# Kernel optimization log

Measured on AMD Instinct MI355X. Metric: run time of the kernel, lower is better.

## Reference

```python
import jax, jax.numpy as jnp
import numpy as np

N, E, G = 16384, 65536, 512
T, FIN, FOUT = 4, 128, 32
_DEG_HIST = np.array([1.0, 2.0, 3.0, 4.0])
AVG_LOG = float((np.log(np.arange(4) + 1.0) * _DEG_HIST).sum() / _DEG_HIST.sum())


def _bn(x, g, b, eps=1e-5):
    # BatchNorm1d in training mode: biased batch stats
    m = x.mean(0)
    v = x.var(0)
    return (x - m) * jax.lax.rsqrt(v + eps) * g + b


def _pna_conv(x, edge_index, ea_raw, We_c, be_c, Wpre, bpre, Wpost, bpost, Wlin, blin):
    src, dst = edge_index[0], edge_index[1]
    ea = ea_raw @ We_c + be_c                                   # conv-internal edge encoder [E,FIN]
    xt = jnp.broadcast_to(x[:, None, :], (N, T, FIN))           # towers share input (divide_input=False)
    h = jnp.concatenate([xt[dst], xt[src],
                         jnp.broadcast_to(ea[:, None, :], (E, T, FIN))], axis=-1)  # [E,T,3*FIN]
    m = jnp.einsum('etf,tfg->etg', h, Wpre) + bpre              # per-tower pre-NN [E,T,FIN]
    deg = jnp.clip(jax.ops.segment_sum(jnp.ones((E,), x.dtype), dst, N), 1.0)
    inv = (1.0 / deg)[:, None, None]
    mean = jax.ops.segment_sum(m, dst, N) * inv
    mean2 = jax.ops.segment_sum(m * m, dst, N) * inv
    std = jnp.sqrt(jax.nn.relu(mean2 - mean * mean) + 1e-5)
    mn = jax.ops.segment_min(m, dst, N)
    mx = jax.ops.segment_max(m, dst, N)
    mn = jnp.where(jnp.isfinite(mn), mn, 0.0)
    mx = jnp.where(jnp.isfinite(mx), mx, 0.0)
    agg = jnp.concatenate([mean, mn, mx, std], axis=-1)         # [N,T,4*FIN]
    s = (jnp.log(deg + 1.0) / AVG_LOG)[:, None, None]           # amplification scaler
    out = jnp.concatenate([agg, agg * s, agg / s], axis=-1)     # identity|amp|attenuation [N,T,12*FIN]
    out = jnp.concatenate([xt, out], axis=-1)                   # [N,T,13*FIN]
    out = jnp.einsum('ntf,tfg->ntg', out, Wpost) + bpost        # per-tower post-NN [N,T,FOUT]
    return out.reshape(N, T * FOUT) @ Wlin + blin               # tower mixing [N,FIN]


def setup_inputs() -> dict:
    key = jax.random.key(0)
    ks = jax.random.split(key, 24)
    def rn(k, shape, scale=0.05):
        return jax.random.normal(k, shape, dtype=jnp.float32) * scale
    return dict(
        x=jax.random.normal(ks[0], (N, 11), jnp.float32),
        edge_attr=jax.random.uniform(ks[1], (E, 4), jnp.float32),
        edge_index=jax.random.randint(ks[2], (2, E), 0, N),
        batch=jnp.sort(jax.random.randint(ks[3], (N,), 0, G)),
        Wa=rn(ks[4], (11, FIN), 0.2), ba=rn(ks[5], (FIN,)),
        We=rn(ks[6], (4, FIN), 0.2), be=rn(ks[7], (FIN,)),
        We_conv=rn(ks[8], (3, FIN, FIN)), be_conv=rn(ks[9], (3, FIN)),
        Wpre=rn(ks[10], (3, T, 3 * FIN, FIN)), bpre=rn(ks[11], (3, T, FIN)),
        Wpost=rn(ks[12], (3, T, 13 * FIN, FOUT)), bpost=rn(ks[13], (3, T, FOUT)),
        Wlin=rn(ks[14], (3, FIN, FIN)), blin=rn(ks[15], (3, FIN)),
        bng=1.0 + rn(ks[16], (3, FIN)), bnb=rn(ks[17], (3, FIN)),
        W1=rn(ks[18], (FIN, 64), 0.1), b1=rn(ks[19], (64,)),
        hg=1.0 + rn(ks[20], (64,)), hb=rn(ks[21], (64,)),
        W2=rn(ks[22], (64, 1), 0.1), b2=rn(ks[23], (1,)),
    )


def reference(x, edge_attr, edge_index, batch, Wa, ba, We, be,
              We_conv, be_conv, Wpre, bpre, Wpost, bpost, Wlin, blin,
              bng, bnb, W1, b1, hg, hb, W2, b2):
    h = jax.nn.relu(x @ Wa + ba)
    ea = jax.nn.relu(edge_attr @ We + be)
    for l in range(3):
        h = jax.nn.relu(_bn(_pna_conv(h, edge_index, ea, We_conv[l], be_conv[l],
                                      Wpre[l], bpre[l], Wpost[l], bpost[l],
                                      Wlin[l], blin[l]), bng[l], bnb[l]))
    cnt = jnp.clip(jax.ops.segment_sum(jnp.ones((N,), h.dtype), batch, G), 1.0)
    pooled = jax.ops.segment_sum(h, batch, G) / cnt[:, None]    # global_mean_pool
    z = jax.nn.relu(pooled @ W1 + b1)
    z = _bn(z, hg, hb)
    return (z @ W2 + b2).reshape(-1)
```

## Files before the change

kernel.cpp:

```cpp
#include <hip/hip_runtime.h>
#include <hip/hip_bf16.h>

#define DEVFN static __device__ __forceinline__

constexpr int NN = 16384;
constexpr int EE = 65536;
constexpr int GG = 512;
constexpr float AVG_LOG_F = 1.0227308671603782f;

typedef _Float16 hfrag __attribute__((ext_vector_type(8)));
typedef __attribute__((ext_vector_type(4))) float f4;

DEVFN unsigned short f2h(float f) {
  _Float16 h = (_Float16)f;
  unsigned short r; __builtin_memcpy(&r, &h, 2); return r;
}
DEVFN float h2f(unsigned short s) {
  _Float16 h; __builtin_memcpy(&h, &s, 2); return (float)h;
}

DEVFN float4 ld4hf(const unsigned short* p) {
  ushort4 u = *(const ushort4*)p;
  float4 r;
  r.x = h2f(u.x); r.y = h2f(u.y); r.z = h2f(u.z); r.w = h2f(u.w);
  return r;
}

DEVFN int swk(int row, int k) {
  return (k & ~31) + ((((k >> 3) & 3) ^ ((row >> 1) & 3)) << 3) + (k & 7);
}

DEVFN void gll16(const unsigned short* g, unsigned short* l) {
  __builtin_amdgcn_global_load_lds(
      (__attribute__((address_space(1))) void*)g,
      (__attribute__((address_space(3))) void*)l, 16, 0, 0);
}

struct AuxP {
  const float* p0;
  const float* p1;
  const float* p2;
  const float* p3;
  const float* p4;
};

template <int ASRC, int NT, bool BIAS, bool RELU, bool OHALF>
__global__ __launch_bounds__(256) void mgemm(
    const void* __restrict__ Av, const unsigned short* __restrict__ WT,
    const float* __restrict__ bias,
    float* __restrict__ C, AuxP aux,
    int Nc, int K, int lda, int ldc,
    long long bsA, long long bsW, long long bsC, int bsBias)
{
  constexpr bool COPYA = (ASRC == 1);
  constexpr int BST = NT * 16 * 32;

  const int z = blockIdx.z;
  WT += (long long)z * bsW;
  if (BIAS) bias += (long long)z * bsBias;
  float* Cf = C + (OHALF ? 0 : (long long)z * bsC);
  unsigned short* Cu = (unsigned short*)C + (OHALF ? (long long)z * bsC : 0);

  __shared__ __align__(16) unsigned short AhS[2 * 128 * 32];
  __shared__ __align__(16) unsigned short BhS[2 * BST];

  const int tid = threadIdx.x;
  const long long bm = (long long)blockIdx.x * 128;
  const int bn = blockIdx.y * (NT * 16);
  const int w = tid >> 6;
  const int lane = tid & 63;
  const int quad = lane >> 4;
  const int c16 = lane & 15;
  const int srow = lane >> 2;
  const int sslot = (lane & 3) << 3;

  const int arow = tid >> 1;
  const int sel = tid & 1;
  const long long rowsrc = bm + arow;

  f4 acc[2][NT];
#pragma unroll
  for (int mt = 0; mt < 2; ++mt)
#pragma unroll
    for (int nt = 0; nt < NT; ++nt) acc[mt][nt] = (f4){0.f, 0.f, 0.f, 0.f};

  const unsigned short* whp = WT + (long long)(bn + srow) * K + sslot;

  const unsigned short* ahp = nullptr;
  if (COPYA || ASRC == 3)
    ahp = (const unsigned short*)Av + (long long)z * bsA + (bm + srow) * (long long)lda + sslot;

  float invdc = 1.f;
  float sv = 0.f, iv = 0.f;
  const float* apA = nullptr;
  const float* Prow_base = nullptr;
  if (ASRC == 3) {
    Prow_base = aux.p0 + rowsrc * 384;
    sv = aux.p2[rowsrc];
    iv = aux.p3[rowsrc];
  } else if (ASRC == 4) {
    apA = (const float*)Av + (long long)z * bsA + rowsrc * lda;
    invdc = 1.f / fmaxf(aux.p0[rowsrc], 1.f);
  }
  const int swa = (arow >> 1) & 3;
  const int s0us = arow * 32 + (((2 * sel) ^ swa) << 3);
  const int s1us = arow * 32 + (((2 * sel + 1) ^ swa) << 3);

  const int swr8 = ((quad ^ ((c16 >> 1) & 3)) << 3);

  auto stageB = [&](int bi, int k0) {
#pragma unroll
    for (int ch = w; ch < NT; ch += 4)
      gll16(whp + (long long)ch * 16 * K + k0, BhS + bi * BST + ch * 512);
  };
  auto stageA = [&](int bi, int k0) {
#pragma unroll
    for (int ch = w; ch < 8; ch += 4)
      gll16(ahp + (long long)ch * 16 * lda + k0, AhS + bi * 4096 + ch * 512);
  };
  auto stageLoad = [&](int k0, float* va) {
    const int ck0 = k0 + sel * 16;
    if (ASRC == 3) {
      const float* Prow = Prow_base + ((ck0 >> 5) * 96) + (ck0 & 31);
#pragma unroll
      for (int i = 0; i < 16; ++i)
        va[i] = Prow[i] + sv * Prow[32 + i] + iv * Prow[64 + i] + aux.p4[ck0 + i];
    } else {
      *(float4*)&va[0] = *(const float4*)(apA + ck0);
      *(float4*)&va[4] = *(const float4*)(apA + ck0 + 4);
      *(float4*)&va[8] = *(const float4*)(apA + ck0 + 8);
      *(float4*)&va[12] = *(const float4*)(apA + ck0 + 12);
    }
  };
  auto stageWrite = [&](int bi, const float* va) {
    hfrag hv0, hv1;
#pragma unroll
    for (int i = 0; i < 16; ++i) {
      float x = va[i];
      if (ASRC == 4) x *= invdc;
      if (i < 8) hv0[i] = (_Float16)x;
      else       hv1[i - 8] = (_Float16)x;
    }
    *(hfrag*)&AhS[bi * 4096 + s0us] = hv0;
    *(hfrag*)&AhS[bi * 4096 + s1us] = hv1;
  };
  auto fragmfma = [&](int bi) {
    hfrag ah[2];
#pragma unroll
    for (int mt = 0; mt < 2; ++mt) {
      const int r = w * 32 + mt * 16 + c16;
      ah[mt] = *(const hfrag*)&AhS[bi * 4096 + r * 32 + swr8];
    }
#pragma unroll
    for (int nt = 0; nt < NT; ++nt) {
      const int r = nt * 16 + c16;
      hfrag bh = *(const hfrag*)&BhS[bi * BST + r * 32 + swr8];
#pragma unroll
      for (int mt = 0; mt < 2; ++mt)
        acc[mt][nt] = __builtin_amdgcn_mfma_f32_16x16x32_f16(ah[mt], bh, acc[mt][nt], 0, 0, 0);
    }
  };

  float va[16];
  const int nk = K >> 5;

  if (COPYA) {
    stageA(0, 0);
    stageB(0, 0);
  } else {
    stageLoad(0, va);
    stageB(0, 0);
    stageWrite(0, va);
  }
  __syncthreads();

  for (int kt = 0; kt < nk; ++kt) {
    const int bi = kt & 1;
    const bool pf = (kt + 1 < nk);
    bool nextds = false;
    if (pf) {
      const int k0 = (kt + 1) << 5;
      stageB(bi ^ 1, k0);
      if (COPYA) {
        stageA(bi ^ 1, k0);
      } else if (ASRC == 3 && k0 >= 128) {
        stageA(bi ^ 1, k0 - 128);
      } else {
        stageLoad(k0, va);
        nextds = true;
      }
    }
    fragmfma(bi);
    if (nextds) stageWrite(bi ^ 1, va);
    __syncthreads();
  }

  float ls[NT], lq[NT];
#pragma unroll
  for (int nt = 0; nt < NT; ++nt) { ls[nt] = 0.f; lq[nt] = 0.f; }
#pragma unroll
  for (int nt = 0; nt < NT; ++nt) {
    int col = bn + nt * 16 + c16;
    if (col >= Nc) continue;
    float bv = BIAS ? bias[col] : 0.f;
#pragma unroll
    for (int mt = 0; mt < 2; ++mt) {
#pragma unroll
      for (int r = 0; r < 4; ++r) {
        long long row = bm + w * 32 + mt * 16 + quad * 4 + r;
        float v = acc[mt][nt][r] + bv;
        if (RELU) v = fmaxf(v, 0.f);
        if (ASRC == 3) { ls[nt] += v; lq[nt] += v * v; }
        if (OHALF) Cu[row * ldc + col] = f2h(v);
        else Cf[row * ldc + col] = v;
      }
    }
  }
  if constexpr (ASRC == 3) {
    float* csum = (float*)AhS;
    float* csq = csum + 128;
    if (tid < 256 && tid >= 128) {}
    if (tid < 128) { csum[tid] = 0.f; csq[tid] = 0.f; }
    __syncthreads();
#pragma unroll
    for (int nt = 0; nt < NT; ++nt) {
      int col = bn + nt * 16 + c16;
      atomicAdd(&csum[col], ls[nt]);
      atomicAdd(&csq[col], lq[nt]);
    }
    __syncthreads();
    float* colsum = (float*)aux.p1;
    if (tid < 128) {
      atomicAdd(&colsum[tid], csum[tid]);
      atomicAdd(&colsum[128 + tid], csq[tid]);
    }
  }
}

__global__ void node_enc(const float* __restrict__ x, const float* __restrict__ Wa,
                         const float* __restrict__ ba, unsigned short* __restrict__ hb)
{
  int n = blockIdx.x, c = threadIdx.x;
  float acc = ba[c];
#pragma unroll
  for (int k = 0; k < 11; ++k) acc += x[n * 11 + k] * Wa[k * 128 + c];
  hb[((long long)n << 7) + swk(n, c)] = f2h(fmaxf(acc, 0.f));
}

__global__ void edge_enc(const float* __restrict__ eat, const float* __restrict__ We,
                         const float* __restrict__ be, const int* __restrict__ slot_of,
                         unsigned short* __restrict__ ef)
{
  int e = blockIdx.x, c = threadIdx.x;
  float acc = be[c];
#pragma unroll
  for (int k = 0; k < 4; ++k) acc += eat[e * 4 + k] * We[k * 128 + c];
  long long slot = slot_of[e];
  ef[slot * 128 + swk((int)slot, c)] = f2h(fmaxf(acc, 0.f));
}

__global__ void count_deg(const int* __restrict__ dst, int* __restrict__ degi)
{
  int e = blockIdx.x * 256 + threadIdx.x;
  if (e < EE) atomicAdd(&degi[dst[e]], 1);
}

__global__ __launch_bounds__(1024) void scan_k(const int* __restrict__ degi,
                                               int* __restrict__ row_off,
                                               int* __restrict__ cursor,
                                               float* __restrict__ s_arr,
                                               float* __restrict__ invs)
{
  __shared__ int tsum[1024];
  int t = threadIdx.x;
  int local[16];
  int base = t * 16;
  int s = 0;
#pragma unroll
  for (int i = 0; i < 16; ++i) { local[i] = s; s += degi[base + i]; }
  tsum[t] = s;
  __syncthreads();
  for (int off = 1; off < 1024; off <<= 1) {
    int v = (t >= off) ? tsum[t - off] : 0;
    __syncthreads();
    tsum[t] += v;
    __syncthreads();
  }
  int prev = (t == 0) ? 0 : tsum[t - 1];
#pragma unroll
  for (int i = 0; i < 16; ++i) {
    int start = prev + local[i];
    row_off[base + i] = start;
    cursor[base + i] = start;
    int cnt = degi[base + i];
    float degc = fmaxf((float)cnt, 1.f);
    float sv = logf(degc + 1.f) / AVG_LOG_F;
    s_arr[base + i] = sv;
    invs[base + i] = 1.f / sv;
  }
  if (t == 1023) row_off[NN] = tsum[1023];
}

__global__ void scatter_k(const int* __restrict__ src, const int* __restrict__ dst,
                          int* __restrict__ cursor,
                          int* __restrict__ slot_of, int* __restrict__ esrc)
{
  int e = blockIdx.x * 256 + threadIdx.x;
  if (e >= EE) return;
  int d = dst[e];
  int slot = atomicAdd(&cursor[d], 1);
  slot_of[e] = slot;
  esrc[slot] = src[e];
}

__global__ __launch_bounds__(512) void fold_w(const float* __restrict__ We_conv,
                                              const float* __restrict__ Wpre,
                                              float* __restrict__ Wfold)
{
  int k = blockIdx.x & 127, l = blockIdx.x >> 7;
  int t = threadIdx.x >> 7, f = threadIdx.x & 127;
  const float* wc = We_conv + (long long)(l * 128 + k) * 128;
  const float* wp = Wpre + ((long long)((l * 4 + t) * 384 + 256)) * 128 + f;
  float acc = 0.f;
  for (int j = 0; j < 128; ++j) acc += wc[j] * wp[(long long)j * 128];
  Wfold[((long long)(l * 128 + k)) * 512 + threadIdx.x] = acc;
}

__global__ __launch_bounds__(512) void fold_b(const float* __restrict__ be_conv,
                                              const float* __restrict__ Wpre,
                                              const float* __restrict__ bpre,
                                              float* __restrict__ bfold)
{
  int l = blockIdx.x;
  int t = threadIdx.x >> 7, f = threadIdx.x & 127;
  const float* bc = be_conv + l * 128;
  const float* wp = Wpre + ((long long)((l * 4 + t) * 384 + 256)) * 128 + f;
  float acc = bpre[(l * 4 + t) * 128 + f];
  for (int j = 0; j < 128; ++j) acc += bc[j] * wp[(long long)j * 128];
  bfold[l * 512 + threadIdx.x] = acc;
}

__global__ __launch_bounds__(128) void pack_all(
    const float* __restrict__ Wpre, const float* __restrict__ WfoldF,
    const float* __restrict__ Wpost, const float* __restrict__ Wlin,
    const float* __restrict__ W1,
    unsigned short* __restrict__ preABT, unsigned short* __restrict__ foldT,
    unsigned short* __restrict__ post3T, unsigned short* __restrict__ linT2,
    unsigned short* __restrict__ w1T)
{
  const int b = blockIdx.x;
  const int t = threadIdx.x;
  if (b < 3072) {
    int lt = b >> 8, n = b & 255, k = t;
    int row = (n < 128) ? k : (128 + k);
    int f = n & 127;
    float v = Wpre[((long long)(lt * 384 + row)) * 128 + f];
    preABT[((long long)(lt * 256 + n)) * 128 + swk(n, k)] = f2h(v);
  } else if (b < 4608) {
    int b2 = b - 3072;
    int lt = b2 >> 7, n = b2 & 127, k = t;
    int l = lt >> 2, tw = lt & 3;
    float v = WfoldF[((long long)(l * 128 + k)) * 512 + tw * 128 + n];
    foldT[((long long)(lt * 128 + n)) * 128 + swk(n, k)] = f2h(v);
  } else if (b < 6144) {
    int b3 = b - 4608;
    int lt = b3 >> 7, c = b3 & 127;
#pragma unroll
    for (int j = 0; j < 4; ++j) {
      int r = t + 128 * j;
      float v = 0.f;
      if (c < 96)
        v = Wpost[((long long)(lt * 1664 + 128 + (c >> 5) * 512 + r)) * 32 + (c & 31)];
      post3T[((long long)(lt * 128 + c)) * 512 + swk(c, r)] = f2h(v);
    }
  } else if (b < 6528) {
    int b4 = b - 6144;
    int l = b4 >> 7, n = b4 & 127, k = t;
    float v = Wlin[((long long)(l * 128 + k)) * 128 + n];
    linT2[((long long)(l * 128 + n)) * 256 + swk(n, k)] = f2h(v);
  } else if (b < 6912) {
    int b5 = b - 6528;
    int l = b5 >> 7, kk = b5 & 127, o = t;
    float acc = 0.f;
    for (int c = 0; c < 128; ++c) {
      float wx = Wpost[((long long)((l * 4 + (c >> 5)) * 1664 + kk)) * 32 + (c & 31)];
      acc += wx * Wlin[((long long)(l * 128 + c)) * 128 + o];
    }
    linT2[((long long)(l * 128 + o)) * 256 + swk(o, 128 + kk)] = f2h(acc);
  } else {
    int n = b - 6912, k = t;
    w1T[(long long)n * 128 + swk(n, k)] = f2h(W1[k * 64 + n]);
  }
}

__global__ __launch_bounds__(256) void aggregate_ct(
    const unsigned short* __restrict__ ABb, const unsigned short* __restrict__ Mb,
    const int* __restrict__ row_off, const int* __restrict__ esrc,
    unsigned short* __restrict__ aggs)
{
  const int tid = threadIdx.x;
  const int c4 = (tid & 31) << 2;
  const int z = (tid >> 5) & 3;
  const int n = blockIdx.x * 2 + (tid >> 7);
  const unsigned short* M = Mb + (long long)z * EE * 128;
  const unsigned short* ABs = ABb + (long long)z * NN * 256;
  unsigned short* ag = aggs + (long long)z * NN * 512;
  const int beg = row_off[n], end = row_off[n + 1];
  const int cnt = end - beg;
  const float degc = fmaxf((float)cnt, 1.0f);
  const float4 aval = ld4hf(&ABs[(long long)n * 256 + c4]);

  float sum[4] = {0.f, 0.f, 0.f, 0.f}, sq[4] = {0.f, 0.f, 0.f, 0.f};
  float mn[4] = {INFINITY, INFINITY, INFINITY, INFINITY};
  float mx[4] = {-INFINITY, -INFINITY, -INFINITY, -INFINITY};

  auto upd = [&](const float4& mv, const float4& bv) {
    float m0 = aval.x + bv.x + mv.x;
    float m1 = aval.y + bv.y + mv.y;
    float m2 = aval.z + bv.z + mv.z;
    float m3 = aval.w + bv.w + mv.w;
    sum[0] += m0; sq[0] += m0 * m0; mn[0] = fminf(mn[0], m0); mx[0] = fmaxf(mx[0], m0);
    sum[1] += m1; sq[1] += m1 * m1; mn[1] = fminf(mn[1], m1); mx[1] = fmaxf(mx[1], m1);
    sum[2] += m2; sq[2] += m2 * m2; mn[2] = fminf(mn[2], m2); mx[2] = fmaxf(mx[2], m2);
    sum[3] += m3; sq[3] += m3 * m3; mn[3] = fminf(mn[3], m3); mx[3] = fmaxf(mx[3], m3);
  };

  for (int s0 = beg; s0 < end; s0 += 4) {
    const int e1 = min(s0 + 1, end - 1);
    const int e2 = min(s0 + 2, end - 1);
    const int e3 = min(s0 + 3, end - 1);
    const int sA = esrc[s0], sB = esrc[e1], sC = esrc[e2], sD = esrc[e3];
    const float4 mA = ld4hf(&M[(long long)s0 * 128 + c4]);
    const float4 mB = ld4hf(&M[(long long)e1 * 128 + c4]);
    const float4 mC = ld4hf(&M[(long long)e2 * 128 + c4]);
    const float4 mD = ld4hf(&M[(long long)e3 * 128 + c4]);
    const float4 bA = ld4hf(&ABs[(long long)sA * 256 + 128 + c4]);
    const float4 bB = ld4hf(&ABs[(long long)sB * 256 + 128 + c4]);
    const float4 bC = ld4hf(&ABs[(long long)sC * 256 + 128 + c4]);
    const float4 bD = ld4hf(&ABs[(long long)sD * 256 + 128 + c4]);
    upd(mA, bA);
    if (s0 + 1 < end) upd(mB, bB);
    if (s0 + 2 < end) upd(mC, bC);
    if (s0 + 3 < end) upd(mD, bD);
  }

  const float inv = 1.0f / degc;
  float mean[4], stdv[4];
#pragma unroll
  for (int j = 0; j < 4; ++j) {
    mean[j] = sum[j] * inv;
    float var = sq[j] * inv - mean[j] * mean[j];
    stdv[j] = sqrtf(fmaxf(var, 0.f) + 1e-5f);
    if (cnt == 0) { mn[j] = 0.f; mx[j] = 0.f; }
  }
  const int sc = swk(n, c4);
  const long long base = (long long)n * 512 + sc;
  ushort4 o;
  o.x = f2h(mean[0]); o.y = f2h(mean[1]); o.z = f2h(mean[2]); o.w = f2h(mean[3]);
  *(ushort4*)&ag[base] = o;
  o.x = f2h(mn[0]); o.y = f2h(mn[1]); o.z = f2h(mn[2]); o.w = f2h(mn[3]);
  *(ushort4*)&ag[base + 128] = o;
  o.x = f2h(mx[0]); o.y = f2h(mx[1]); o.z = f2h(mx[2]); o.w = f2h(mx[3]);
  *(ushort4*)&ag[base + 256] = o;
  o.x = f2h(stdv[0]); o.y = f2h(stdv[1]); o.z = f2h(stdv[2]); o.w = f2h(stdv[3]);
  *(ushort4*)&ag[base + 384] = o;
}

__global__ void bn_coef(const float* __restrict__ colsum, const float* __restrict__ colsq,
                        const float* __restrict__ g, const float* __restrict__ b,
                        float* __restrict__ coef)
{
  int c = threadIdx.x;
  float mean = colsum[c] * (1.f / 16384.f);
  float var = colsq[c] * (1.f / 16384.f) - mean * mean;
  float sc = g[c] * rsqrtf(var + 1e-5f);
  coef[c] = sc;
  coef[128 + c] = b[c] - mean * sc;
}

__global__ __launch_bounds__(256) void bn_apply(const float* __restrict__ y,
                                                const float* __restrict__ coef,
                                                unsigned short* __restrict__ hb)
{
  int idx = blockIdx.x * 256 + threadIdx.x;
  int c = idx & 127, n = idx >> 7;
  float v = fmaxf(y[idx] * coef[c] + coef[128 + c], 0.f);
  hb[((long long)n << 7) + swk(n, c)] = f2h(v);
}

__global__ void pool_add(const float* __restrict__ y, const float* __restrict__ colsum,
                         const float* __restrict__ colsq, const float* __restrict__ g,
                         const float* __restrict__ b, const int* __restrict__ batch,
                         float* __restrict__ pooled, float* __restrict__ cntf)
{
  int n = blockIdx.x, c = threadIdx.x;
  float mean = colsum[c] * (1.f / 16384.f);
  float var = colsq[c] * (1.f / 16384.f) - mean * mean;
  float v = fmaxf((y[(long long)n * 128 + c] - mean) * rsqrtf(var + 1e-5f) * g[c] + b[c], 0.f);
  int bb = batch[n];
  atomicAdd(&pooled[(long long)bb * 128 + c], v);
  if (c == 0) atomicAdd(&cntf[bb], 1.f);
}

__global__ __launch_bounds__(256) void zstats(const float* __restrict__ z,
                                              float* __restrict__ zm, float* __restrict__ zv)
{
  int j = blockIdx.x;
  float s = 0.f, q = 0.f;
  for (int g = threadIdx.x; g < GG; g += 256) {
    float v = z[g * 64 + j];
    s += v;
    q += v * v;
  }
  __shared__ float ps[256], pq[256];
  ps[threadIdx.x] = s;
  pq[threadIdx.x] = q;
  __syncthreads();
  for (int st = 128; st > 0; st >>= 1) {
    if (threadIdx.x < st) {
      ps[threadIdx.x] += ps[threadIdx.x + st];
      pq[threadIdx.x] += pq[threadIdx.x + st];
    }
    __syncthreads();
  }
  if (threadIdx.x == 0) {
    float m = ps[0] / (float)GG;
    zm[j] = m;
    zv[j] = pq[0] / (float)GG - m * m;
  }
}

__global__ void final_out(const float* __restrict__ z, const float* __restrict__ zm,
                          const float* __restrict__ zv, const float* __restrict__ hg,
                          const float* __restrict__ hb, const float* __restrict__ W2,
                          const float* __restrict__ b2, float* __restrict__ out)
{
  int g = blockIdx.x;
  int j = threadIdx.x;
  float v = (z[g * 64 + j] - zm[j]) * rsqrtf(zv[j] + 1e-5f) * hg[j] + hb[j];
  float t = v * W2[j];
#pragma unroll
  for (int off = 32; off > 0; off >>= 1) t += __shfl_down(t, off);
  if (j == 0) out[g] = t + b2[0];
}

extern "C" void kernel_launch(void* const* d_in, const int* in_sizes, int n_in,
                              void* d_out, int out_size, void* d_ws, size_t ws_size,
                              hipStream_t stream)
{
  (void)in_sizes; (void)n_in; (void)out_size;
  const float* x = (const float*)d_in[0];
  const float* eat = (const float*)d_in[1];
  const int* ei = (const int*)d_in[2];
  const int* batch = (const int*)d_in[3];
  const float* Wa = (const float*)d_in[4];
  const float* ba = (const float*)d_in[5];
  const float* We = (const float*)d_in[6];
  const float* be = (const float*)d_in[7];
  const float* We_conv = (const float*)d_in[8];
  const float* be_conv = (const float*)d_in[9];
  const float* Wpre = (const float*)d_in[10];
  const float* bpre = (const float*)d_in[11];
  const float* Wpost = (const float*)d_in[12];
  const float* bpost = (const float*)d_in[13];
  const float* Wlin = (const float*)d_in[14];
  const float* blin = (const float*)d_in[15];
  const float* bng = (const float*)d_in[16];
  const float* bnb = (const float*)d_in[17];
  const float* W1 = (const float*)d_in[18];
  const float* b1 = (const float*)d_in[19];
  const float* hg = (const float*)d_in[20];
  const float* hb = (const float*)d_in[21];
  const float* W2 = (const float*)d_in[22];
  const float* b2 = (const float*)d_in[23];
  float* out = (float*)d_out;

  const int* srcI = ei;
  const int* dstI = ei + EE;

  char* ws = (char*)d_ws;
  size_t off = 0;
  auto alloc = [&](size_t bytes) -> char* {
    char* p = ws + off;
    off += (bytes + 255) & ~(size_t)255;
    return p;
  };

  unsigned short* hbf = (unsigned short*)alloc((size_t)NN * 128 * 2);
  float* hn = (float*)alloc((size_t)NN * 128 * 4);
  unsigned short* eaf = (unsigned short*)alloc((size_t)EE * 128 * 2);
  unsigned short* AB = (unsigned short*)alloc((size_t)4 * NN * 256 * 2);
  char* Mregion = alloc((size_t)4 * EE * 128 * 2);
  unsigned short* Mb = (unsigned short*)Mregion;
  float* P = (float*)Mregion;
  unsigned short* aggt = (unsigned short*)alloc((size_t)4 * NN * 512 * 2);
  float* s_arr = (float*)alloc((size_t)NN * 4);
  float* invs = (float*)alloc((size_t)NN * 4);
  int* degi = (int*)alloc((size_t)NN * 4);
  int* cursor = (int*)alloc((size_t)NN * 4);
  int* row_off = (int*)alloc((size_t)(NN + 1) * 4);
  int* slot_of = (int*)alloc((size_t)EE * 4);
  int* esrc = (int*)alloc((size_t)EE * 4);
  float* WfoldF = (float*)alloc((size_t)3 * 128 * 512 * 4);
  float* bfold = (float*)alloc((size_t)3 * 512 * 4);
  unsigned short* preABT = (unsigned short*)alloc((size_t)12 * 256 * 128 * 2);
  unsigned short* foldT = (unsigned short*)alloc((size_t)12 * 128 * 128 * 2);
  unsigned short* post3T = (unsigned short*)alloc((size_t)12 * 128 * 512 * 2);
  unsigned short* linT2 = (unsigned short*)alloc((size_t)3 * 128 * 256 * 2);
  unsigned short* w1T = (unsigned short*)alloc((size_t)64 * 128 * 2);
  float* colstats = (float*)alloc(512 * 4);
  float* bncoef = (float*)alloc(256 * 4);
  float* pooled = (float*)alloc((size_t)GG * 128 * 4);
  float* cntf = (float*)alloc((size_t)GG * 4);
  float* zbuf = (float*)alloc((size_t)GG * 64 * 4);
  float* zm = (float*)alloc(64 * 4);
  float* zv = (float*)alloc(64 * 4);

  if (off > ws_size) return;

  float* cs[2] = {colstats, colstats + 256};

  hipMemsetAsync(degi, 0, (size_t)NN * 4, stream);
  count_deg<<<EE / 256, 256, 0, stream>>>(dstI, degi);
  scan_k<<<1, 1024, 0, stream>>>(degi, row_off, cursor, s_arr, invs);
  scatter_k<<<EE / 256, 256, 0, stream>>>(srcI, dstI, cursor, slot_of, esrc);

  node_enc<<<NN, 128, 0, stream>>>(x, Wa, ba, hbf);
  edge_enc<<<EE, 128, 0, stream>>>(eat, We, be, slot_of, eaf);
  fold_w<<<384, 512, 0, stream>>>(We_conv, Wpre, WfoldF);
  fold_b<<<3, 512, 0, stream>>>(be_conv, Wpre, bpre, bfold);
  pack_all<<<6976, 128, 0, stream>>>(Wpre, WfoldF, Wpost, Wlin, W1,
                                     preABT, foldT, post3T, linT2, w1T);

  for (int l = 0; l < 3; ++l) {
    hipMemsetAsync(cs[l & 1], 0, 256 * 4, stream);
    mgemm<1, 8, false, false, true><<<dim3(NN / 128, 2, 4), 256, 0, stream>>>(
        hbf, preABT + (size_t)l * 4 * 256 * 128, nullptr, (float*)AB, AuxP{},
        256, 128, 128, 256, 0, (long long)256 * 128, (long long)NN * 256, 0);
    mgemm<1, 8, true, false, true><<<dim3(EE / 128, 1, 4), 256, 0, stream>>>(
        eaf, foldT + (size_t)l * 4 * 128 * 128, bfold + l * 512, (float*)Mb, AuxP{},
        128, 128, 128, 128, 0, (long long)128 * 128, (long long)EE * 128, 128);
    aggregate_ct<<<dim3(NN / 2, 1, 1), 256, 0, stream>>>(AB, Mb, row_off, esrc, aggt);
    mgemm<1, 6, false, false, false><<<dim3(NN / 128, 1, 4), 256, 0, stream>>>(
        aggt, post3T + (size_t)l * 4 * 128 * 512, nullptr, P, AuxP{},
        96, 512, 512, 384, (long long)NN * 512, (long long)128 * 512, 96, 0);
    mgemm<3, 8, true, false, false><<<dim3(NN / 128, 1, 1), 256, 0, stream>>>(
        hbf, linT2 + (size_t)l * 128 * 256, blin + l * 128, hn,
        AuxP{P, cs[l & 1], s_arr, invs, bpost + l * 128},
        128, 256, 128, 128, 0, 0, 0, 0);
    if (l < 2) {
      bn_coef<<<1, 128, 0, stream>>>(cs[l & 1], cs[l & 1] + 128,
                                     bng + l * 128, bnb + l * 128, bncoef);
      bn_apply<<<NN * 128 / 256, 256, 0, stream>>>(hn, bncoef, hbf);
    }
  }

  hipMemsetAsync(pooled, 0, (size_t)GG * 128 * 4, stream);
  hipMemsetAsync(cntf, 0, (size_t)GG * 4, stream);
  pool_add<<<NN, 128, 0, stream>>>(hn, cs[0], cs[0] + 128,
                                   bng + 2 * 128, bnb + 2 * 128, batch, pooled, cntf);
  mgemm<4, 4, true, true, false><<<dim3(GG / 128, 1, 1), 256, 0, stream>>>(
      pooled, w1T, b1, zbuf, AuxP{cntf, nullptr, nullptr, nullptr, nullptr},
      64, 128, 128, 64, 0, 0, 0, 0);
  zstats<<<64, 256, 0, stream>>>(zbuf, zm, zv);
  final_out<<<GG, 64, 0, stream>>>(zbuf, zm, zv, hg, hb, W2, b2, out);
}
```

Baseline: 596.7 us.

## Merge pre-GEMMs, fold node encoder into pack, store intermediates in fp16, inline BN coef

Combines the node-projection and edge-projection GEMMs of each layer into one launch (abc_gemm) with a block-index split. Moves the node encoder into the pack_all kernel and packs two edges per block in edge_enc. Stores the post-GEMM output P and the layer output hn as fp16 instead of fp32, which halves that traffic. Also computes the BN coefficients inside bn_apply and zeroes all colstats with a single memset, removing kernel launches. The fp16 intermediates add rounding error before batch norm.

After: 570.0 us. 1.05x faster.

```diff
diff --git a/kernel.cpp b/kernel.cpp
--- a/kernel.cpp
+++ b/kernel.cpp
@@ -43,6 +43,102 @@
   const float* p3;
   const float* p4;
 };
+
+__global__ __launch_bounds__(256) void abc_gemm(
+    const unsigned short* __restrict__ hbf, const unsigned short* __restrict__ preABT_l,
+    unsigned short* __restrict__ AB,
+    const unsigned short* __restrict__ eaf, const unsigned short* __restrict__ foldT_l,
+    const float* __restrict__ bfold_l, unsigned short* __restrict__ Mb)
+{
+  __shared__ __align__(16) unsigned short AhS[2 * 4096];
+  __shared__ __align__(16) unsigned short BhS[2 * 4096];
+
+  const int bid = blockIdx.x;
+  const unsigned short* Abase;
+  const unsigned short* Wbase;
+  const float* bias = nullptr;
+  unsigned short* Cu;
+  int ldc, bn;
+  long long bm;
+  if (bid < 1024) {
+    const int z = bid >> 8, y = (bid >> 7) & 1, xm = bid & 127;
+    Abase = hbf;
+    Wbase = preABT_l + (size_t)z * 256 * 128;
+    Cu = AB + (size_t)z * NN * 256;
+    ldc = 256; bn = y * 128; bm = (long long)xm * 128;
+  } else {
+    const int idx = bid - 1024;
+    const int z = idx >> 9, xm = idx & 511;
+    Abase = eaf;
+    Wbase = foldT_l + (size_t)z * 128 * 128;
+    bias = bfold_l + z * 128;
+    Cu = Mb + (size_t)z * EE * 128;
+    ldc = 128; bn = 0; bm = (long long)xm * 128;
+  }
+
+  const int tid = threadIdx.x;
+  const int w = tid >> 6;
+  const int lane = tid & 63;
+  const int quad = lane >> 4;
+  const int c16 = lane & 15;
+  const int srow = lane >> 2;
+  const int sslot = (lane & 3) << 3;
+
+  f4 acc[2][8];
+#pragma unroll
+  for (int mt = 0; mt < 2; ++mt)
+#pragma unroll
+    for (int nt = 0; nt < 8; ++nt) acc[mt][nt] = (f4){0.f, 0.f, 0.f, 0.f};
+
+  const unsigned short* whp = Wbase + (long long)(bn + srow) * 128 + sslot;
+  const unsigned short* ahp = Abase + (bm + srow) * 128 + sslot;
+  const int swr8 = ((quad ^ ((c16 >> 1) & 3)) << 3);
+
+  auto stage = [&](int bi, int k0) {
+#pragma unroll
+    for (int ch = w; ch < 8; ch += 4) {
+      gll16(ahp + (long long)ch * 16 * 128 + k0, AhS + bi * 4096 + ch * 512);
+      gll16(whp + (long long)ch * 16 * 128 + k0, BhS + bi * 4096 + ch * 512);
+    }
+  };
+  auto fragmfma = [&](int bi) {
+    hfrag ah[2];
+#pragma unroll
+    for (int mt = 0; mt < 2; ++mt)
+      ah[mt] = *(const hfrag*)&AhS[bi * 4096 + (w * 32 + mt * 16 + c16) * 32 + swr8];
+#pragma unroll
+    for (int nt = 0; nt < 8; ++nt) {
+      hfrag bh = *(const hfrag*)&BhS[bi * 4096 + (nt * 16 + c16) * 32 + swr8];
+#pragma unroll
+      for (int mt = 0; mt < 2; ++mt)
+        acc[mt][nt] = __builtin_amdgcn_mfma_f32_16x16x32_f16(ah[mt], bh, acc[mt][nt], 0, 0, 0);
+    }
+  };
+
+  stage(0, 0);
+  __syncthreads();
+#pragma unroll
+  for (int kt = 0; kt < 4; ++kt) {
+    const int bi = kt & 1;
+    if (kt < 3) stage(bi ^ 1, (kt + 1) << 5);
+    fragmfma(bi);
+    __syncthreads();
+  }
+
+#pragma unroll
+  for (int nt = 0; nt < 8; ++nt) {
+    const int col = bn + nt * 16 + c16;
+    const float bv = bias ? bias[nt * 16 + c16] : 0.f;
+#pragma unroll
+    for (int mt = 0; mt < 2; ++mt) {
+#pragma unroll
+      for (int r = 0; r < 4; ++r) {
+        long long row = bm + w * 32 + mt * 16 + quad * 4 + r;
+        Cu[row * ldc + col] = f2h(acc[mt][nt][r] + bv);
+      }
+    }
+  }
+}
 
 template <int ASRC, int NT, bool BIAS, bool RELU, bool OHALF>
 __global__ __launch_bounds__(256) void mgemm(
@@ -93,9 +189,9 @@
   float invdc = 1.f;
   float sv = 0.f, iv = 0.f;
   const float* apA = nullptr;
-  const float* Prow_base = nullptr;
+  const unsigned short* Prow_base = nullptr;
   if (ASRC == 3) {
-    Prow_base = aux.p0 + rowsrc * 384;
+    Prow_base = (const unsigned short*)aux.p0 + rowsrc * 384;
     sv = aux.p2[rowsrc];
     iv = aux.p3[rowsrc];
   } else if (ASRC == 4) {
@@ -121,10 +217,22 @@
   auto stageLoad = [&](int k0, float* va) {
     const int ck0 = k0 + sel * 16;
     if (ASRC == 3) {
-      const float* Prow = Prow_base + ((ck0 >> 5) * 96) + (ck0 & 31);
+      const unsigned short* Prow = Prow_base + ((ck0 >> 5) * 96) + (ck0 & 31);
+      float4 pid0 = ld4hf(Prow), pid1 = ld4hf(Prow + 4);
+      float4 pid2 = ld4hf(Prow + 8), pid3 = ld4hf(Prow + 12);
+      float4 pam0 = ld4hf(Prow + 32), pam1 = ld4hf(Prow + 36);
+      float4 pam2 = ld4hf(Prow + 40), pam3 = ld4hf(Prow + 44);
+      float4 pat0 = ld4hf(Prow + 64), pat1 = ld4hf(Prow + 68);
+      float4 pat2 = ld4hf(Prow + 72), pat3 = ld4hf(Prow + 76);
+      float pid[16] = {pid0.x, pid0.y, pid0.z, pid0.w, pid1.x, pid1.y, pid1.z, pid1.w,
+                       pid2.x, pid2.y, pid2.z, pid2.w, pid3.x, pid3.y, pid3.z, pid3.w};
+      float pam[16] = {pam0.x, pam0.y, pam0.z, pam0.w, pam1.x, pam1.y, pam1.z, pam1.w,
+                       pam2.x, pam2.y, pam2.z, pam2.w, pam3.x, pam3.y, pam3.z, pam3.w};
+      float pat[16] = {pat0.x, pat0.y, pat0.z, pat0.w, pat1.x, pat1.y, pat1.z, pat1.w,
+                       pat2.x, pat2.y, pat2.z, pat2.w, pat3.x, pat3.y, pat3.z, pat3.w};
 #pragma unroll
       for (int i = 0; i < 16; ++i)
-        va[i] = Prow[i] + sv * Prow[32 + i] + iv * Prow[64 + i] + aux.p4[ck0 + i];
+        va[i] = pid[i] + sv * pam[i] + iv * pat[i] + aux.p4[ck0 + i];
     } else {
       *(float4*)&va[0] = *(const float4*)(apA + ck0);
       *(float4*)&va[4] = *(const float4*)(apA + ck0 + 4);
@@ -219,7 +327,6 @@
   if constexpr (ASRC == 3) {
     float* csum = (float*)AhS;
     float* csq = csum + 128;
-    if (tid < 256 && tid >= 128) {}
     if (tid < 128) { csum[tid] = 0.f; csq[tid] = 0.f; }
     __syncthreads();
 #pragma unroll
@@ -237,21 +344,13 @@
   }
 }
 
-__global__ void node_enc(const float* __restrict__ x, const float* __restrict__ Wa,
-                         const float* __restrict__ ba, unsigned short* __restrict__ hb)
-{
-  int n = blockIdx.x, c = threadIdx.x;
-  float acc = ba[c];
-#pragma unroll
-  for (int k = 0; k < 11; ++k) acc += x[n * 11 + k] * Wa[k * 128 + c];
-  hb[((long long)n << 7) + swk(n, c)] = f2h(fmaxf(acc, 0.f));
-}
-
-__global__ void edge_enc(const float* __restrict__ eat, const float* __restrict__ We,
-                         const float* __restrict__ be, const int* __restrict__ slot_of,
-                         unsigned short* __restrict__ ef)
-{
-  int e = blockIdx.x, c = threadIdx.x;
+__global__ __launch_bounds__(256) void edge_enc(
+    const float* __restrict__ eat, const float* __restrict__ We,
+    const float* __restrict__ be, const int* __restrict__ slot_of,
+    unsigned short* __restrict__ ef)
+{
+  int e = blockIdx.x * 2 + (threadIdx.x >> 7);
+  int c = threadIdx.x & 127;
   float acc = be[c];
 #pragma unroll
   for (int k = 0; k < 4; ++k) acc += eat[e * 4 + k] * We[k * 128 + c];
@@ -344,9 +443,11 @@
     const float* __restrict__ Wpre, const float* __restrict__ WfoldF,
     const float* __restrict__ Wpost, const float* __restrict__ Wlin,
     const float* __restrict__ W1,
+    const float* __restrict__ x, const float* __restrict__ Wa,
+    const float* __restrict__ ba,
     unsigned short* __restrict__ preABT, unsigned short* __restrict__ foldT,
     unsigned short* __restrict__ post3T, unsigned short* __restrict__ linT2,
-    unsigned short* __restrict__ w1T)
+    unsigned short* __restrict__ w1T, unsigned short* __restrict__ hbf)
 {
   const int b = blockIdx.x;
   const int t = threadIdx.x;
@@ -387,9 +488,15 @@
       acc += wx * Wlin[((long long)(l * 128 + c)) * 128 + o];
     }
     linT2[((long long)(l * 128 + o)) * 256 + swk(o, 128 + kk)] = f2h(acc);
-  } else {
+  } else if (b < 6976) {
     int n = b - 6912, k = t;
     w1T[(long long)n * 128 + swk(n, k)] = f2h(W1[k * 64 + n]);
+  } else {
+    int n = b - 6976, c = t;
+    float acc = ba[c];
+#pragma unroll
+    for (int k = 0; k < 11; ++k) acc += x[n * 11 + k] * Wa[k * 128 + c];
+    hbf[((long long)n << 7) + swk(n, c)] = f2h(fmaxf(acc, 0.f));
   }
 }
 
@@ -466,37 +573,30 @@
   *(ushort4*)&ag[base + 384] = o;
 }
 
-__global__ void bn_coef(const float* __restrict__ colsum, const float* __restrict__ colsq,
-                        const float* __restrict__ g, const float* __restrict__ b,
-                        float* __restrict__ coef)
-{
-  int c = threadIdx.x;
-  float mean = colsum[c] * (1.f / 16384.f);
-  float var = colsq[c] * (1.f / 16384.f) - mean * mean;
-  float sc = g[c] * rsqrtf(var + 1e-5f);
-  coef[c] = sc;
-  coef[128 + c] = b[c] - mean * sc;
-}
-
-__global__ __launch_bounds__(256) void bn_apply(const float* __restrict__ y,
-                                                const float* __restrict__ coef,
+__global__ __launch_bounds__(256) void bn_apply(const unsigned short* __restrict__ hn,
+                                                const float* __restrict__ cs,
+                                                const float* __restrict__ g,
+                                                const float* __restrict__ b,
                                                 unsigned short* __restrict__ hb)
 {
   int idx = blockIdx.x * 256 + threadIdx.x;
   int c = idx & 127, n = idx >> 7;
-  float v = fmaxf(y[idx] * coef[c] + coef[128 + c], 0.f);
+  float mean = cs[c] * (1.f / 16384.f);
+  float var = cs[128 + c] * (1.f / 16384.f) - mean * mean;
+  float sc = g[c] * rsqrtf(var + 1e-5f);
+  float v = fmaxf(h2f(hn[idx]) * sc + (b[c] - mean * sc), 0.f);
   hb[((long long)n << 7) + swk(n, c)] = f2h(v);
 }
 
-__global__ void pool_add(const float* __restrict__ y, const float* __restrict__ colsum,
-                         const float* __restrict__ colsq, const float* __restrict__ g,
-                         const float* __restrict__ b, const int* __restrict__ batch,
+__global__ void pool_add(const unsigned short* __restrict__ y, const float* __restrict__ cs,
+                         const float* __restrict__ g, const float* __restrict__ b,
+                         const int* __restrict__ batch,
                          float* __restrict__ pooled, float* __restrict__ cntf)
 {
   int n = blockIdx.x, c = threadIdx.x;
-  float mean = colsum[c] * (1.f / 16384.f);
-  float var = colsq[c] * (1.f / 16384.f) - mean * mean;
-  float v = fmaxf((y[(long long)n * 128 + c] - mean) * rsqrtf(var + 1e-5f) * g[c] + b[c], 0.f);
+  float mean = cs[c] * (1.f / 16384.f);
+  float var = cs[128 + c] * (1.f / 16384.f) - mean * mean;
+  float v = fmaxf((h2f(y[(long long)n * 128 + c]) - mean) * rsqrtf(var + 1e-5f) * g[c] + b[c], 0.f);
   int bb = batch[n];
   atomicAdd(&pooled[(long long)bb * 128 + c], v);
   if (c == 0) atomicAdd(&cntf[bb], 1.f);
@@ -587,12 +687,12 @@
   };
 
   unsigned short* hbf = (unsigned short*)alloc((size_t)NN * 128 * 2);
-  float* hn = (float*)alloc((size_t)NN * 128 * 4);
+  unsigned short* hn = (unsigned short*)alloc((size_t)NN * 128 * 2);
   unsigned short* eaf = (unsigned short*)alloc((size_t)EE * 128 * 2);
   unsigned short* AB = (unsigned short*)alloc((size_t)4 * NN * 256 * 2);
   char* Mregion = alloc((size_t)4 * EE * 128 * 2);
   unsigned short* Mb = (unsigned short*)Mregion;
-  float* P = (float*)Mregion;
+  unsigned short* P = (unsigned short*)Mregion;
   unsigned short* aggt = (unsigned short*)alloc((size_t)4 * NN * 512 * 2);
   float* s_arr = (float*)alloc((size_t)NN * 4);
   float* invs = (float*)alloc((size_t)NN * 4);
@@ -608,8 +708,7 @@
   unsigned short* post3T = (unsigned short*)alloc((size_t)12 * 128 * 512 * 2);
   unsigned short* linT2 = (unsigned short*)alloc((size_t)3 * 128 * 256 * 2);
   unsigned short* w1T = (unsigned short*)alloc((size_t)64 * 128 * 2);
-  float* colstats = (float*)alloc(512 * 4);
-  float* bncoef = (float*)alloc(256 * 4);
+  float* colstats = (float*)alloc(3 * 256 * 4);
   float* pooled = (float*)alloc((size_t)GG * 128 * 4);
   float* cntf = (float*)alloc((size_t)GG * 4);
   float* zbuf = (float*)alloc((size_t)GG * 64 * 4);
@@ -618,46 +717,39 @@
 
   if (off > ws_size) return;
 
-  float* cs[2] = {colstats, colstats + 256};
-
   hipMemsetAsync(degi, 0, (size_t)NN * 4, stream);
+  hipMemsetAsync(colstats, 0, 3 * 256 * 4, stream);
   count_deg<<<EE / 256, 256, 0, stream>>>(dstI, degi);
   scan_k<<<1, 1024, 0, stream>>>(degi, row_off, cursor, s_arr, invs);
   scatter_k<<<EE / 256, 256, 0, stream>>>(srcI, dstI, cursor, slot_of, esrc);
 
-  node_enc<<<NN, 128, 0, stream>>>(x, Wa, ba, hbf);
-  edge_enc<<<EE, 128, 0, stream>>>(eat, We, be, slot_of, eaf);
+  edge_enc<<<EE / 2, 256, 0, stream>>>(eat, We, be, slot_of, eaf);
   fold_w<<<384, 512, 0, stream>>>(We_conv, Wpre, WfoldF);
   fold_b<<<3, 512, 0, stream>>>(be_conv, Wpre, bpre, bfold);
-  pack_all<<<6976, 128, 0, stream>>>(Wpre, WfoldF, Wpost, Wlin, W1,
-                                     preABT, foldT, post3T, linT2, w1T);
+  pack_all<<<6976 + NN, 128, 0, stream>>>(Wpre, WfoldF, Wpost, Wlin, W1, x, Wa, ba,
+                                          preABT, foldT, post3T, linT2, w1T, hbf);
 
   for (int l = 0; l < 3; ++l) {
-    hipMemsetAsync(cs[l & 1], 0, 256 * 4, stream);
-    mgemm<1, 8, false, false, true><<<dim3(NN / 128, 2, 4), 256, 0, stream>>>(
-        hbf, preABT + (size_t)l * 4 * 256 * 128, nullptr, (float*)AB, AuxP{},
-        256, 128, 128, 256, 0, (long long)256 * 128, (long long)NN * 256, 0);
-    mgemm<1, 8, true, false, true><<<dim3(EE / 128, 1, 4), 256, 0, stream>>>(
-        eaf, foldT + (size_t)l * 4 * 128 * 128, bfold + l * 512, (float*)Mb, AuxP{},
-        128, 128, 128, 128, 0, (long long)128 * 128, (long long)EE * 128, 128);
+    float* cs_l = colstats + l * 256;
+    abc_gemm<<<3072, 256, 0, stream>>>(
+        hbf, preABT + (size_t)l * 4 * 256 * 128, AB,
+        eaf, foldT + (size_t)l * 4 * 128 * 128, bfold + l * 512, Mb);
     aggregate_ct<<<dim3(NN / 2, 1, 1), 256, 0, stream>>>(AB, Mb, row_off, esrc, aggt);
-    mgemm<1, 6, false, false, false><<<dim3(NN / 128, 1, 4), 256, 0, stream>>>(
-        aggt, post3T + (size_t)l * 4 * 128 * 512, nullptr, P, AuxP{},
+    mgemm<1, 6, false, false, true><<<dim3(NN / 128, 1, 4), 256, 0, stream>>>(
+        aggt, post3T + (size_t)l * 4 * 128 * 512, nullptr, (float*)P, AuxP{},
         96, 512, 512, 384, (long long)NN * 512, (long long)128 * 512, 96, 0);
-    mgemm<3, 8, true, false, false><<<dim3(NN / 128, 1, 1), 256, 0, stream>>>(
-        hbf, linT2 + (size_t)l * 128 * 256, blin + l * 128, hn,
-        AuxP{P, cs[l & 1], s_arr, invs, bpost + l * 128},
+    mgemm<3, 8, true, false, true><<<dim3(NN / 128, 1, 1), 256, 0, stream>>>(
+        hbf, linT2 + (size_t)l * 128 * 256, blin + l * 128, (float*)hn,
+        AuxP{(const float*)P, cs_l, s_arr, invs, bpost + l * 128},
         128, 256, 128, 128, 0, 0, 0, 0);
-    if (l < 2) {
-      bn_coef<<<1, 128, 0, stream>>>(cs[l & 1], cs[l & 1] + 128,
-                                     bng + l * 128, bnb + l * 128, bncoef);
-      bn_apply<<<NN * 128 / 256, 256, 0, stream>>>(hn, bncoef, hbf);
-    }
+    if (l < 2)
+      bn_apply<<<NN * 128 / 256, 256, 0, stream>>>(hn, cs_l, bng + l * 128,
+                                                   bnb + l * 128, hbf);
   }
 
   hipMemsetAsync(pooled, 0, (size_t)GG * 128 * 4, stream);
   hipMemsetAsync(cntf, 0, (size_t)GG * 4, stream);
-  pool_add<<<NN, 128, 0, stream>>>(hn, cs[0], cs[0] + 128,
+  pool_add<<<NN, 128, 0, stream>>>(hn, colstats + 2 * 256,
                                    bng + 2 * 128, bnb + 2 * 128, batch, pooled, cntf);
   mgemm<4, 4, true, true, false><<<dim3(GG / 128, 1, 1), 256, 0, stream>>>(
       pooled, w1T, b1, zbuf, AuxP{cntf, nullptr, nullptr, nullptr, nullptr},
```
